# Optimization experiments

Hardware: AMD Instinct MI355X
Metric: run time of the kernel (lower is better)

Reference implementation:

```python
import jax, jax.numpy as jnp
import numpy as np

NUM_HEADS = 8


def setup_inputs() -> dict:
    key = jax.random.key(0)
    ks = jax.random.split(key, 6)
    B, E, L = 8, 256, 4096
    top_k = 256
    return {
        "query": jax.random.normal(ks[0], (B, E, L), jnp.float32),
        "keys": jax.random.normal(ks[1], (B, E, L), jnp.float32),
        "values": jax.random.normal(ks[2], (B, E, L), jnp.float32),
        "rand_token_ind": jax.random.randint(ks[3], (B, top_k), 0, L),
        "in_proj_weight": jax.random.normal(ks[4], (3 * E, E), jnp.float32) / np.float32(np.sqrt(E)),
        "in_proj_bias": jnp.zeros((3 * E,), jnp.float32),
        "out_proj_weight": jax.random.normal(ks[5], (E, E), jnp.float32) / np.float32(np.sqrt(E)),
        "out_proj_bias": jnp.zeros((E,), jnp.float32),
        "top_k": top_k,
    }


def _forward(query, keys, values, rand_token_ind, in_proj_weight, in_proj_bias,
             out_proj_weight, out_proj_bias, top_k):
    B, E, Lq = query.shape
    # flatten(2).transpose(-1,-2): channel-first -> [B, L, E]
    q = jnp.swapaxes(query, 1, 2)
    k = jnp.swapaxes(keys, 1, 2)
    v = jnp.swapaxes(values, 1, 2)

    # --- dist_to_random_Q_selection ---
    # random subset of queries, [B, S, E]
    Q_small = jnp.take_along_axis(q, rand_token_ind[:, :, None], axis=1)

    # running min over subset queries of L1 distance (avoids [B,Lk,S,D] blowup)
    def step(min_d, qs):  # qs: [B, E]
        d = jnp.sum(jnp.abs(k - qs[:, None, :]), axis=-1)  # [B, Lk]
        return jnp.minimum(min_d, d), None

    init = jnp.full((B, k.shape[1]), jnp.inf, dtype=k.dtype)
    min_d, _ = jax.lax.scan(step, init, jnp.swapaxes(Q_small, 0, 1))

    # top_k smallest distances, sorted ascending (torch largest=False, sorted=True)
    _, idx = jax.lax.top_k(-min_d, top_k)  # idx: [B, top_k]
    sk = jnp.take_along_axis(k, idx[:, :, None], axis=1)  # [B, top_k, E]
    sv = jnp.take_along_axis(v, idx[:, :, None], axis=1)

    # --- standard torch MultiheadAttention (batch_first) ---
    Wq, Wk, Wv = jnp.split(in_proj_weight, 3, axis=0)
    bq, bk, bv = jnp.split(in_proj_bias, 3, axis=0)
    hd = E // NUM_HEADS
    scale = hd ** -0.5

    def heads(x):
        return x.reshape(x.shape[0], x.shape[1], NUM_HEADS, hd)

    qh = heads(q @ Wq.T + bq) * scale      # [B, Lq, H, hd]
    kh = heads(sk @ Wk.T + bk)             # [B, K,  H, hd]
    vh = heads(sv @ Wv.T + bv)

    scores = jnp.einsum('bqhd,bkhd->bhqk', qh, kh)
    attn = jax.nn.softmax(scores, axis=-1)
    o = jnp.einsum('bhqk,bkhd->bqhd', attn, vh).reshape(B, Lq, E)
    out = o @ out_proj_weight.T + out_proj_bias  # [B, Lq, E]

    # transpose back to original [B, E, Lq] layout
    return jnp.swapaxes(out, 1, 2)


def reference(query, keys, values, rand_token_ind, in_proj_weight, in_proj_bias,
              out_proj_weight, out_proj_bias, top_k):
    return _forward(query, keys, values, rand_token_ind, in_proj_weight,
                    in_proj_bias, out_proj_weight, out_proj_bias, top_k)
```

## Files before the change

### kernel.cpp

```cpp
#include <hip/hip_runtime.h>
#include <math.h>

#define B_SZ   8
#define E_DIM  256
#define L_SEQ  4096
#define S_TOP  256
#define NHEAD  8
#define HD     32
#define NSPLIT 4
#define JSPL   8

typedef __attribute__((ext_vector_type(8))) short bf16x8;
typedef __attribute__((ext_vector_type(4))) float f32x4;

__device__ inline short f2bf(float x) {
    union { float f; unsigned u; } v; v.f = x;
    unsigned r = (v.u + 0x7fff + ((v.u >> 16) & 1)) >> 16;
    return (short)r;
}

__global__ __launch_bounds__(256) void k_gather(const float* __restrict__ query,
                                                const int* __restrict__ ind,
                                                float* __restrict__ qs_pack) {
    int t = blockIdx.x * 256 + threadIdx.x;
    int e = t & (E_DIM - 1);
    int s = (t >> 8) & (S_TOP - 1);
    int b = t >> 16;
    int idx = ind[b * S_TOP + s];
    qs_pack[t] = query[((size_t)b * E_DIM + e) * L_SEQ + idx];
}

__global__ __launch_bounds__(256) void k_dist(const float* __restrict__ keys,
                                              const float* __restrict__ qs_pack,
                                              double* __restrict__ minpart) {
    const int b    = blockIdx.z;
    const int ss   = blockIdx.y;
    const int l0   = blockIdx.x * 64;
    const int lane = threadIdx.x;
    const int sg   = threadIdx.y;
    const int lid  = sg * 64 + lane;
    __shared__ float  Ks[32][64];
    __shared__ float  Qs[64][36];
    __shared__ double red[4][64];
    const float* kb = keys + (size_t)b * E_DIM * L_SEQ + l0;
    const float* qb = qs_pack + ((size_t)b * S_TOP + ss * 64) * E_DIM;

    double d[16];
#pragma unroll
    for (int j = 0; j < 16; ++j) d[j] = 0.0;

    for (int c0 = 0; c0 < E_DIM; c0 += 32) {
        __syncthreads();
#pragma unroll
        for (int r = 0; r < 2; ++r) {
            int f4 = lid + 256 * r;
            int e  = f4 >> 4, l4 = (f4 & 15) * 4;
            *(float4*)&Ks[e][l4] = *(const float4*)(kb + (size_t)(c0 + e) * L_SEQ + l4);
            int s  = f4 >> 3, e4 = (f4 & 7) * 4;
            *(float4*)&Qs[s][e4] = *(const float4*)(qb + (size_t)s * E_DIM + c0 + e4);
        }
        __syncthreads();
        float kr[32];
#pragma unroll
        for (int e = 0; e < 32; ++e) kr[e] = Ks[e][lane];
#pragma unroll
        for (int si = 0; si < 16; ++si) {
            const float* qrow = &Qs[sg * 16 + si][0];
            float csum = 0.f;
#pragma unroll
            for (int e = 0; e < 32; ++e) csum += fabsf(kr[e] - qrow[e]);
            d[si] += (double)csum;
        }
    }
    double md = d[0];
#pragma unroll
    for (int j = 1; j < 16; ++j) md = fmin(md, d[j]);
    red[sg][lane] = md;
    __syncthreads();
    if (sg == 0) {
        double m = red[0][lane];
        m = fmin(m, red[1][lane]);
        m = fmin(m, red[2][lane]);
        m = fmin(m, red[3][lane]);
        minpart[((size_t)(b * NSPLIT + ss)) * L_SEQ + l0 + lane] = m;
    }
}

__global__ __launch_bounds__(256) void k_rankpart(const double* __restrict__ minpart,
                                                  int* __restrict__ rankpart) {
    const int b  = blockIdx.z;
    const int js = blockIdx.y;
    const int l  = blockIdx.x * 256 + threadIdx.x;
    __shared__ double sd[512];
    const double* mp = minpart + (size_t)b * NSPLIT * L_SEQ;
    for (int jj = threadIdx.x; jj < 512; jj += 256) {
        const int j = js * 512 + jj;
        double v = mp[j];
        v = fmin(v, mp[L_SEQ + j]);
        v = fmin(v, mp[2 * L_SEQ + j]);
        v = fmin(v, mp[3 * L_SEQ + j]);
        sd[jj] = v;
    }
    double dl = mp[l];
    dl = fmin(dl, mp[L_SEQ + l]);
    dl = fmin(dl, mp[2 * L_SEQ + l]);
    dl = fmin(dl, mp[3 * L_SEQ + l]);
    __syncthreads();
    const int jbase = js * 512;
    int rank = 0;
#pragma unroll 8
    for (int jj = 0; jj < 512; ++jj) {
        double dj = sd[jj];
        rank += (dj < dl) || (dj == dl && (jbase + jj) < l) ? 1 : 0;
    }
    rankpart[((size_t)(b * JSPL + js)) * L_SEQ + l] = rank;
}

__global__ __launch_bounds__(256) void k_sel(const int* __restrict__ rankpart,
                                             int* __restrict__ sel) {
    const int t = blockIdx.x * 256 + threadIdx.x;
    const int b = t >> 12;
    const int l = t & (L_SEQ - 1);
    int r = 0;
#pragma unroll
    for (int s = 0; s < JSPL; ++s)
        r += rankpart[((size_t)(b * JSPL + s)) * L_SEQ + l];
    if (r < S_TOP) sel[b * S_TOP + r] = l;
}

__global__ __launch_bounds__(256) void k_kvproj2(const float* __restrict__ keys,
                                                 const float* __restrict__ vals,
                                                 const int* __restrict__ sel,
                                                 const float* __restrict__ Wk,
                                                 const float* __restrict__ bk,
                                                 const float* __restrict__ Wv,
                                                 const float* __restrict__ bv,
                                                 short* __restrict__ khb,
                                                 short* __restrict__ vtb) {
    const int b  = blockIdx.z;
    const int f0 = blockIdx.x * 64;
    const int TR = blockIdx.y >> 2;
    const int k0 = (blockIdx.y & 3) * 64;
    const float* src  = TR ? vals : keys;
    const float* W    = TR ? Wv : Wk;
    const float* bias = TR ? bv : bk;
    const int tx = threadIdx.x, ty = threadIdx.y;
    const int lid = ty * 16 + tx;
    __shared__ float As[16][68];
    __shared__ float Ws[16][68];
    float c[4][4] = {};
    const float* sb = src + (size_t)b * E_DIM * L_SEQ;
    const int* selb = sel + b * S_TOP;
    for (int e0 = 0; e0 < E_DIM; e0 += 16) {
        {
            int e  = lid >> 4;
            int k4 = (lid & 15) * 4;
#pragma unroll
            for (int c2 = 0; c2 < 4; ++c2) {
                int kk = k4 + c2;
                As[e][kk] = sb[(size_t)(e0 + e) * L_SEQ + selb[k0 + kk]];
            }
        }
        {
            int f  = lid >> 2;
            int e4 = (lid & 3) * 4;
            float4 w = *(const float4*)(W + (size_t)(f0 + f) * E_DIM + e0 + e4);
            Ws[e4 + 0][f] = w.x; Ws[e4 + 1][f] = w.y;
            Ws[e4 + 2][f] = w.z; Ws[e4 + 3][f] = w.w;
        }
        __syncthreads();
#pragma unroll
        for (int e = 0; e < 16; ++e) {
            float4 a = *(const float4*)&As[e][ty * 4];
            float4 w = *(const float4*)&Ws[e][tx * 4];
            float av[4] = {a.x, a.y, a.z, a.w};
            float wv[4] = {w.x, w.y, w.z, w.w};
#pragma unroll
            for (int i = 0; i < 4; ++i)
#pragma unroll
                for (int j = 0; j < 4; ++j) c[i][j] += av[i] * wv[j];
        }
        __syncthreads();
    }
    if (TR == 0) {
#pragma unroll
        for (int i = 0; i < 4; ++i) {
            short4 o;
            o.x = f2bf(c[i][0] + bias[f0 + tx * 4 + 0]);
            o.y = f2bf(c[i][1] + bias[f0 + tx * 4 + 1]);
            o.z = f2bf(c[i][2] + bias[f0 + tx * 4 + 2]);
            o.w = f2bf(c[i][3] + bias[f0 + tx * 4 + 3]);
            *(short4*)(khb + ((size_t)b * S_TOP + k0 + ty * 4 + i) * E_DIM + f0 + tx * 4) = o;
        }
    } else {
#pragma unroll
        for (int j = 0; j < 4; ++j) {
            const float bvv = bias[f0 + tx * 4 + j];
            short4 o;
            o.x = f2bf(c[0][j] + bvv); o.y = f2bf(c[1][j] + bvv);
            o.z = f2bf(c[2][j] + bvv); o.w = f2bf(c[3][j] + bvv);
            *(short4*)(vtb + ((size_t)b * E_DIM + f0 + tx * 4 + j) * S_TOP + k0 + ty * 4) = o;
        }
    }
}

__global__ __launch_bounds__(256) void k_qproj(const float* __restrict__ query,
                                               const float* __restrict__ W,
                                               const float* __restrict__ bias,
                                               short* __restrict__ qhb,
                                               float scale) {
    const int b  = blockIdx.z;
    const int f0 = blockIdx.x * 128;
    const int l0 = blockIdx.y * 128;
    const int tx = threadIdx.x, ty = threadIdx.y;
    const int lid = ty * 16 + tx;
    __shared__ float As[16][132];
    __shared__ float Ws[16][132];
    float c[8][8] = {};
    const float* sb = query + (size_t)b * E_DIM * L_SEQ + l0;
    for (int e0 = 0; e0 < E_DIM; e0 += 16) {
        __syncthreads();
#pragma unroll
        for (int r = 0; r < 2; ++r) {
            int f4 = lid + 256 * r;
            int e  = f4 >> 5, l4 = (f4 & 31) * 4;
            *(float4*)&As[e][l4] = *(const float4*)(sb + (size_t)(e0 + e) * L_SEQ + l4);
            int f  = f4 >> 2, e4 = (f4 & 3) * 4;
            float4 w = *(const float4*)(W + (size_t)(f0 + f) * E_DIM + e0 + e4);
            Ws[e4 + 0][f] = w.x; Ws[e4 + 1][f] = w.y;
            Ws[e4 + 2][f] = w.z; Ws[e4 + 3][f] = w.w;
        }
        __syncthreads();
#pragma unroll
        for (int e = 0; e < 16; ++e) {
            float4 a0 = *(const float4*)&As[e][tx * 4];
            float4 a1 = *(const float4*)&As[e][64 + tx * 4];
            float4 w0 = *(const float4*)&Ws[e][ty * 4];
            float4 w1 = *(const float4*)&Ws[e][64 + ty * 4];
            float av[8] = {a0.x, a0.y, a0.z, a0.w, a1.x, a1.y, a1.z, a1.w};
            float wv[8] = {w0.x, w0.y, w0.z, w0.w, w1.x, w1.y, w1.z, w1.w};
#pragma unroll
            for (int i = 0; i < 8; ++i)
#pragma unroll
                for (int j = 0; j < 8; ++j) c[i][j] += av[i] * wv[j];
        }
    }
    float bv[8];
#pragma unroll
    for (int j = 0; j < 8; ++j)
        bv[j] = bias[f0 + ((j < 4) ? ty * 4 + j : 64 + ty * 4 + (j - 4))];
#pragma unroll
    for (int i = 0; i < 8; ++i) {
        const int l = l0 + ((i < 4) ? tx * 4 + i : 64 + tx * 4 + (i - 4));
        short* row = qhb + ((size_t)b * L_SEQ + l) * E_DIM + f0;
        short4 o0, o1;
        o0.x = f2bf(scale * (c[i][0] + bv[0]));
        o0.y = f2bf(scale * (c[i][1] + bv[1]));
        o0.z = f2bf(scale * (c[i][2] + bv[2]));
        o0.w = f2bf(scale * (c[i][3] + bv[3]));
        o1.x = f2bf(scale * (c[i][4] + bv[4]));
        o1.y = f2bf(scale * (c[i][5] + bv[5]));
        o1.z = f2bf(scale * (c[i][6] + bv[6]));
        o1.w = f2bf(scale * (c[i][7] + bv[7]));
        *(short4*)(row + ty * 4) = o0;
        *(short4*)(row + 64 + ty * 4) = o1;
    }
}

__global__ __launch_bounds__(256) void k_attn(const short* __restrict__ qhb,
                                              const short* __restrict__ khb,
                                              const short* __restrict__ vtb,
                                              float* __restrict__ ob) {
    __shared__ short P[4][16][264];
    const int b = blockIdx.z, h = blockIdx.y;
    const int wv   = threadIdx.x >> 6;
    const int lane = threadIdx.x & 63;
    const int quad = lane >> 4;
    const int m    = lane & 15;
    const int l0 = blockIdx.x * 64 + wv * 16;

    const short* qp = qhb + ((size_t)b * L_SEQ + l0 + m) * E_DIM + h * HD + quad * 8;
    const bf16x8 qa = *(const bf16x8*)qp;

    const short* kb = khb + (size_t)b * S_TOP * E_DIM + h * HD + quad * 8;
    f32x4 sacc[16];
    const f32x4 zero = {0.f, 0.f, 0.f, 0.f};
#pragma unroll
    for (int t = 0; t < 16; ++t) {
        bf16x8 kf = *(const bf16x8*)(kb + (size_t)(t * 16 + m) * E_DIM);
        sacc[t] = __builtin_amdgcn_mfma_f32_16x16x32_bf16(qa, kf, zero, 0, 0, 0);
    }

    float mx[4], ssum[4];
#pragma unroll
    for (int r = 0; r < 4; ++r) {
        float v = sacc[0][r];
#pragma unroll
        for (int t = 1; t < 16; ++t) v = fmaxf(v, sacc[t][r]);
#pragma unroll
        for (int off = 1; off < 16; off <<= 1) v = fmaxf(v, __shfl_xor(v, off, 16));
        mx[r] = v;
        ssum[r] = 0.f;
    }
#pragma unroll
    for (int t = 0; t < 16; ++t) {
#pragma unroll
        for (int r = 0; r < 4; ++r) {
            float p = __expf(sacc[t][r] - mx[r]);
            ssum[r] += p;
            P[wv][quad * 4 + r][t * 16 + m] = f2bf(p);
        }
    }
#pragma unroll
    for (int r = 0; r < 4; ++r) {
        float v = ssum[r];
#pragma unroll
        for (int off = 1; off < 16; off <<= 1) v += __shfl_xor(v, off, 16);
        ssum[r] = v;
    }

    const short* vb = vtb + ((size_t)b * E_DIM + h * HD) * S_TOP;
    f32x4 oacc[2];
#pragma unroll
    for (int dt = 0; dt < 2; ++dt) {
        f32x4 acc = zero;
#pragma unroll
        for (int k0 = 0; k0 < S_TOP; k0 += 32) {
            bf16x8 pa = *(const bf16x8*)&P[wv][m][k0 + quad * 8];
            bf16x8 vf = *(const bf16x8*)(vb + (size_t)(dt * 16 + m) * S_TOP + k0 + quad * 8);
            acc = __builtin_amdgcn_mfma_f32_16x16x32_bf16(pa, vf, acc, 0, 0, 0);
        }
        oacc[dt] = acc;
    }

    float* op = ob + ((size_t)b * L_SEQ + l0) * E_DIM + h * HD;
#pragma unroll
    for (int r = 0; r < 4; ++r) {
        const float inv = 1.0f / ssum[r];
#pragma unroll
        for (int dt = 0; dt < 2; ++dt)
            op[(size_t)(quad * 4 + r) * E_DIM + dt * 16 + m] = oacc[dt][r] * inv;
    }
}

__global__ __launch_bounds__(256) void k_outproj(const float* __restrict__ ob,
                                                 const float* __restrict__ W,
                                                 const float* __restrict__ bias,
                                                 float* __restrict__ out) {
    const int b  = blockIdx.z;
    const int l0 = blockIdx.x * 128;
    const int f0 = blockIdx.y * 128;
    const int tx = threadIdx.x, ty = threadIdx.y;
    const int lid = ty * 16 + tx;
    __shared__ float As[16][132];
    __shared__ float Ws[16][132];
    float c[8][8] = {};
    const float* sb = ob + (size_t)b * L_SEQ * E_DIM;
    for (int e0 = 0; e0 < E_DIM; e0 += 16) {
        __syncthreads();
#pragma unroll
        for (int r = 0; r < 2; ++r) {
            int f4 = lid + 256 * r;
            int l  = f4 >> 2, e4 = (f4 & 3) * 4;
            float4 a = *(const float4*)(sb + (size_t)(l0 + l) * E_DIM + e0 + e4);
            As[e4 + 0][l] = a.x; As[e4 + 1][l] = a.y;
            As[e4 + 2][l] = a.z; As[e4 + 3][l] = a.w;
            float4 w = *(const float4*)(W + (size_t)(f0 + l) * E_DIM + e0 + e4);
            Ws[e4 + 0][l] = w.x; Ws[e4 + 1][l] = w.y;
            Ws[e4 + 2][l] = w.z; Ws[e4 + 3][l] = w.w;
        }
        __syncthreads();
#pragma unroll
        for (int e = 0; e < 16; ++e) {
            float4 a0 = *(const float4*)&As[e][tx * 4];
            float4 a1 = *(const float4*)&As[e][64 + tx * 4];
            float4 w0 = *(const float4*)&Ws[e][ty * 4];
            float4 w1 = *(const float4*)&Ws[e][64 + ty * 4];
            float av[8] = {a0.x, a0.y, a0.z, a0.w, a1.x, a1.y, a1.z, a1.w};
            float wv[8] = {w0.x, w0.y, w0.z, w0.w, w1.x, w1.y, w1.z, w1.w};
#pragma unroll
            for (int i = 0; i < 8; ++i)
#pragma unroll
                for (int j = 0; j < 8; ++j) c[i][j] += wv[i] * av[j];
        }
    }
#pragma unroll
    for (int i = 0; i < 8; ++i) {
        const int f = f0 + ((i < 4) ? ty * 4 + i : 64 + ty * 4 + (i - 4));
        const float bvv = bias[f];
        float* row = out + ((size_t)b * E_DIM + f) * L_SEQ + l0;
        float4 o0, o1;
        o0.x = c[i][0] + bvv; o0.y = c[i][1] + bvv;
        o0.z = c[i][2] + bvv; o0.w = c[i][3] + bvv;
        o1.x = c[i][4] + bvv; o1.y = c[i][5] + bvv;
        o1.z = c[i][6] + bvv; o1.w = c[i][7] + bvv;
        *(float4*)(row + tx * 4) = o0;
        *(float4*)(row + 64 + tx * 4) = o1;
    }
}

extern "C" void kernel_launch(void* const* d_in, const int* in_sizes, int n_in,
                              void* d_out, int out_size, void* d_ws, size_t ws_size,
                              hipStream_t stream) {
    const float* query = (const float*)d_in[0];
    const float* keys  = (const float*)d_in[1];
    const float* vals  = (const float*)d_in[2];
    const int*   rind  = (const int*)d_in[3];
    const float* ipw   = (const float*)d_in[4];
    const float* ipb   = (const float*)d_in[5];
    const float* opw   = (const float*)d_in[6];
    const float* opb   = (const float*)d_in[7];
    float* out = (float*)d_out;

    char* ws = (char*)d_ws;
    float*  qs_pack  = (float*)(ws + 0);
    double* minpart  = (double*)(ws + (size_t)2  * 1024 * 1024);
    int*    sel      = (int*)   (ws + (size_t)3  * 1024 * 1024);
    short*  khb      = (short*) (ws + (size_t)4  * 1024 * 1024);
    int*    rankpart = (int*)   (ws + (size_t)5  * 1024 * 1024);
    short*  vtb      = (short*) (ws + (size_t)6  * 1024 * 1024);
    short*  qhb      = (short*) (ws + (size_t)8  * 1024 * 1024);
    float*  obuf     = (float*) (ws + (size_t)40 * 1024 * 1024);

    const float scale = 0.17677669529663687f;

    k_gather<<<dim3((B_SZ * E_DIM * S_TOP) / 256), 256, 0, stream>>>(query, rind, qs_pack);
    k_dist<<<dim3(L_SEQ / 64, NSPLIT, B_SZ), dim3(64, 4), 0, stream>>>(keys, qs_pack, minpart);
    k_rankpart<<<dim3(L_SEQ / 256, JSPL, B_SZ), 256, 0, stream>>>(minpart, rankpart);
    k_sel<<<dim3((B_SZ * L_SEQ) / 256), 256, 0, stream>>>(rankpart, sel);
    k_kvproj2<<<dim3(E_DIM / 64, 2 * (S_TOP / 64), B_SZ), dim3(16, 16), 0, stream>>>(
        keys, vals, sel,
        ipw + (size_t)E_DIM * E_DIM, ipb + E_DIM,
        ipw + (size_t)2 * E_DIM * E_DIM, ipb + 2 * E_DIM,
        khb, vtb);
    k_qproj<<<dim3(E_DIM / 128, L_SEQ / 128, B_SZ), dim3(16, 16), 0, stream>>>(
        query, ipw, ipb, qhb, scale);
    k_attn<<<dim3(L_SEQ / 64, NHEAD, B_SZ), 256, 0, stream>>>(qhb, khb, vtb, obuf);
    k_outproj<<<dim3(L_SEQ / 128, E_DIM / 128, B_SZ), dim3(16, 16), 0, stream>>>(
        obuf, opw, opb, out);
}
```

Measured before the change: 516.5 us.

## Register-tile L1 distance kernel with 4x4 key-query blocking per thread

The distance kernel now gives each thread a 4x4 tile of keys and subset queries instead of one key and 16 queries. Query rows are read as float4 from shared memory and reused across four keys, and key values are reused across four queries. This cuts shared-memory loads per abs-diff operation in the dominant compute loop. The reduction buffer now aliases the key tile in shared memory and reduces over 16 row groups. Per-chunk partial sums are still promoted to double as before, though the order of float additions changes.

New measurement: 495.4 us. 4.1% less time.

```diff
diff --git a/kernel.cpp b/kernel.cpp
--- a/kernel.cpp
+++ b/kernel.cpp
@@ -33,21 +33,24 @@
 __global__ __launch_bounds__(256) void k_dist(const float* __restrict__ keys,
                                               const float* __restrict__ qs_pack,
                                               double* __restrict__ minpart) {
-    const int b    = blockIdx.z;
-    const int ss   = blockIdx.y;
-    const int l0   = blockIdx.x * 64;
-    const int lane = threadIdx.x;
-    const int sg   = threadIdx.y;
-    const int lid  = sg * 64 + lane;
-    __shared__ float  Ks[32][64];
-    __shared__ float  Qs[64][36];
-    __shared__ double red[4][64];
+    const int b  = blockIdx.z;
+    const int ss = blockIdx.y;
+    const int l0 = blockIdx.x * 64;
+    const int lid = threadIdx.x;
+    const int tx = lid & 15;
+    const int ty = lid >> 4;
+    __shared__ float Ks[32][64];
+    __shared__ float Qs[64][36];
+    double (*red)[64] = (double(*)[64])&Ks[0][0];
+
     const float* kb = keys + (size_t)b * E_DIM * L_SEQ + l0;
     const float* qb = qs_pack + ((size_t)b * S_TOP + ss * 64) * E_DIM;
 
-    double d[16];
-#pragma unroll
-    for (int j = 0; j < 16; ++j) d[j] = 0.0;
+    double d[4][4];
+#pragma unroll
+    for (int i = 0; i < 4; ++i)
+#pragma unroll
+        for (int j = 0; j < 4; ++j) d[i][j] = 0.0;
 
     for (int c0 = 0; c0 < E_DIM; c0 += 32) {
         __syncthreads();
@@ -60,29 +63,52 @@
             *(float4*)&Qs[s][e4] = *(const float4*)(qb + (size_t)s * E_DIM + c0 + e4);
         }
         __syncthreads();
-        float kr[32];
-#pragma unroll
-        for (int e = 0; e < 32; ++e) kr[e] = Ks[e][lane];
-#pragma unroll
-        for (int si = 0; si < 16; ++si) {
-            const float* qrow = &Qs[sg * 16 + si][0];
-            float csum = 0.f;
-#pragma unroll
-            for (int e = 0; e < 32; ++e) csum += fabsf(kr[e] - qrow[e]);
-            d[si] += (double)csum;
-        }
-    }
-    double md = d[0];
-#pragma unroll
-    for (int j = 1; j < 16; ++j) md = fmin(md, d[j]);
-    red[sg][lane] = md;
+
+        float cs[4][4] = {};
+#pragma unroll
+        for (int e4 = 0; e4 < 32; e4 += 4) {
+            float qv[4][4];
+#pragma unroll
+            for (int j = 0; j < 4; ++j) {
+                float4 q = *(const float4*)&Qs[ty * 4 + j][e4];
+                qv[j][0] = q.x; qv[j][1] = q.y; qv[j][2] = q.z; qv[j][3] = q.w;
+            }
+#pragma unroll
+            for (int ee = 0; ee < 4; ++ee) {
+                float kv[4];
+#pragma unroll
+                for (int i = 0; i < 4; ++i) kv[i] = Ks[e4 + ee][tx * 4 + i];
+#pragma unroll
+                for (int i = 0; i < 4; ++i)
+#pragma unroll
+                    for (int j = 0; j < 4; ++j)
+                        cs[i][j] += fabsf(kv[i] - qv[j][ee]);
+            }
+        }
+#pragma unroll
+        for (int i = 0; i < 4; ++i)
+#pragma unroll
+            for (int j = 0; j < 4; ++j) d[i][j] += (double)cs[i][j];
+    }
+
+    double md[4];
+#pragma unroll
+    for (int i = 0; i < 4; ++i) {
+        double m = d[i][0];
+        m = fmin(m, d[i][1]);
+        m = fmin(m, d[i][2]);
+        m = fmin(m, d[i][3]);
+        md[i] = m;
+    }
     __syncthreads();
-    if (sg == 0) {
-        double m = red[0][lane];
-        m = fmin(m, red[1][lane]);
-        m = fmin(m, red[2][lane]);
-        m = fmin(m, red[3][lane]);
-        minpart[((size_t)(b * NSPLIT + ss)) * L_SEQ + l0 + lane] = m;
+#pragma unroll
+    for (int i = 0; i < 4; ++i) red[ty][tx * 4 + i] = md[i];
+    __syncthreads();
+    if (lid < 64) {
+        double m = red[0][lid];
+#pragma unroll
+        for (int t = 1; t < 16; ++t) m = fmin(m, red[t][lid]);
+        minpart[((size_t)(b * NSPLIT + ss)) * L_SEQ + l0 + lid] = m;
     }
 }
 
@@ -425,7 +451,7 @@
     const float scale = 0.17677669529663687f;
 
     k_gather<<<dim3((B_SZ * E_DIM * S_TOP) / 256), 256, 0, stream>>>(query, rind, qs_pack);
-    k_dist<<<dim3(L_SEQ / 64, NSPLIT, B_SZ), dim3(64, 4), 0, stream>>>(keys, qs_pack, minpart);
+    k_dist<<<dim3(L_SEQ / 64, NSPLIT, B_SZ), dim3(256), 0, stream>>>(keys, qs_pack, minpart);
     k_rankpart<<<dim3(L_SEQ / 256, JSPL, B_SZ), 256, 0, stream>>>(minpart, rankpart);
     k_sel<<<dim3((B_SZ * L_SEQ) / 256), 256, 0, stream>>>(rankpart, sel);
     k_kvproj2<<<dim3(E_DIM / 64, 2 * (S_TOP / 64), B_SZ), dim3(16, 16), 0, stream>>>(
```
